# Kernel tuning notes

Hardware: AMD Instinct MI355X
Metric: run time of the kernel (lower is better)

The kernel has to match this reference:

```python
import jax, jax.numpy as jnp
import numpy as np
from jax import lax

FEAT_STRIDE = 16
SCALES = (8, 16, 32)
RATIOS = (0.5, 1.0, 2.0)
PRE_NMS = 6000
POST_NMS = 300
NMS_THRESH = 0.7
MIN_SIZE = 16.0


def _base_anchors():
    base = 16.0
    cx = cy = base / 2.0
    anchors = []
    for r in RATIOS:
        for s in SCALES:
            h = base * s * np.sqrt(r)
            w = base * s * np.sqrt(1.0 / r)
            anchors.append([cx - w / 2, cy - h / 2, cx + w / 2, cy + h / 2])
    return np.asarray(anchors, np.float32)  # [A,4] (x1,y1,x2,y2)


def _shifted_anchors(h, w):
    base = _base_anchors()
    sy = np.arange(h, dtype=np.float32) * FEAT_STRIDE
    sx = np.arange(w, dtype=np.float32) * FEAT_STRIDE
    yy, xx = np.meshgrid(sy, sx, indexing='ij')  # h-major then w, matching NHWC permute
    shifts = np.stack([xx, yy, xx, yy], axis=-1).reshape(-1, 1, 4)
    return (shifts + base[None]).reshape(-1, 4).astype(np.float32)  # [h*w*A,4]


def _conv(x, w, b, pad):
    y = lax.conv_general_dilated(x, w, (1, 1), [(pad, pad), (pad, pad)],
                                 dimension_numbers=('NCHW', 'OIHW', 'NCHW'))
    return y + b[None, :, None, None]


def _iou(box, boxes):
    lt = jnp.maximum(box[:2], boxes[:, :2])
    rb = jnp.minimum(box[2:], boxes[:, 2:])
    wh = jnp.maximum(rb - lt, 0.0)
    inter = wh[:, 0] * wh[:, 1]
    a1 = (box[2] - box[0]) * (box[3] - box[1])
    a2 = (boxes[:, 2] - boxes[:, 0]) * (boxes[:, 3] - boxes[:, 1])
    return inter / (a1 + a2 - inter + 1e-9)


def _nms_proposals(boxes, scores):
    # boxes [K,4], scores [K] -> [POST_NMS,4]
    ws = boxes[:, 2] - boxes[:, 0]
    hs = boxes[:, 3] - boxes[:, 1]
    scores = jnp.where((ws >= MIN_SIZE) & (hs >= MIN_SIZE), scores, -jnp.inf)
    top_s, idx = lax.top_k(scores, PRE_NMS)
    b = boxes[idx]

    def body(i, st):
        keep, s = st
        j = jnp.argmax(s).astype(jnp.int32)
        keep = keep.at[i].set(j)
        sup = _iou(b[j], b) >= NMS_THRESH  # suppresses j itself too (iou=1)
        s = jnp.where(sup, -jnp.inf, s)
        return keep, s

    keep, _ = lax.fori_loop(0, POST_NMS, body,
                            (jnp.zeros((POST_NMS,), jnp.int32), top_s))
    return b[keep]


def setup_inputs() -> dict:
    key = jax.random.key(0)
    ks = jax.random.split(key, 5)
    n, c, h, w = 8, 512, 50, 64
    A = len(SCALES) * len(RATIOS)
    x = jax.random.normal(ks[0], (n, c, h, w), jnp.float32)
    w1 = jax.random.normal(ks[1], (512, 512, 3, 3), jnp.float32) * 0.02
    b1 = jnp.zeros((512,), jnp.float32)
    w_cls = jax.random.normal(ks[2], (A * 2, 512, 1, 1), jnp.float32) * 0.02
    b_cls = jnp.zeros((A * 2,), jnp.float32)
    w_bbox = jax.random.normal(ks[3], (A * 4, 512, 1, 1), jnp.float32) * 0.005
    b_bbox = jnp.zeros((A * 4,), jnp.float32)
    return {'x': x, 'w1': w1, 'b1': b1, 'w_cls': w_cls, 'b_cls': b_cls,
            'w_bbox': w_bbox, 'b_bbox': b_bbox}


def reference(x, w1, b1, w_cls, b_cls, w_bbox, b_bbox):
    n, _, h, w = x.shape
    A = len(SCALES) * len(RATIOS)
    img_h, img_w = h * FEAT_STRIDE, w * FEAT_STRIDE
    anchors = jnp.asarray(_shifted_anchors(h, w))  # [h*w*A,4]

    feat = jax.nn.relu(_conv(x, w1, b1, 1))
    cls = _conv(feat, w_cls, b_cls, 0).transpose(0, 2, 3, 1).reshape(n, h, w, A, 2)
    fg = jax.nn.softmax(cls, axis=-1)[..., 1].reshape(n, -1)  # [n, h*w*A]
    deltas = _conv(feat, w_bbox, b_bbox, 0).transpose(0, 2, 3, 1).reshape(n, -1, 4)

    # decode deltas against anchors
    aw = anchors[:, 2] - anchors[:, 0]
    ah = anchors[:, 3] - anchors[:, 1]
    acx = anchors[:, 0] + 0.5 * aw
    acy = anchors[:, 1] + 0.5 * ah
    cx = deltas[..., 0] * aw + acx
    cy = deltas[..., 1] * ah + acy
    pw = jnp.exp(deltas[..., 2]) * aw
    ph = jnp.exp(deltas[..., 3]) * ah
    boxes = jnp.stack([cx - 0.5 * pw, cy - 0.5 * ph,
                       cx + 0.5 * pw, cy + 0.5 * ph], axis=-1)  # [n,K,4]
    hi = jnp.asarray([img_w, img_h, img_w, img_h], jnp.float32)
    boxes = jnp.clip(boxes, 0.0, hi)

    rois = jax.vmap(_nms_proposals)(boxes, fg)  # [n,POST_NMS,4]
    roi_indices = jnp.repeat(jnp.arange(n, dtype=jnp.int32), POST_NMS)
    return rois.reshape(-1, 4), roi_indices
```

## Files before the change

### kernel.cpp

```cpp
#include <hip/hip_runtime.h>
#include <math.h>

#define NIMG 8
#define CIN  512
#define HF   50
#define WF   64
#define HW   3200
#define NA   9
#define KPER 28800
#define PRE  6000
#define POST 300

#define WHT_ELEMS  32768

#define NW    94
#define NCAP  6016
#define NTRI  4465

#define XTROWS 52
#define XTCOLS 66
#define XT_ELEMS ((size_t)NIMG * XTROWS * XTCOLS * CIN)
#define XT_BYTES (XT_ELEMS * 2)

#define WPK_ELEMS ((size_t)2 * 4 * 9 * 16 * 4096)
#define WPK_HALF  (4 * 9 * 16 * 4096)

#define SCALE_X 256.0f
#define SCALE_W 16384.0f
#define INV_SCALE (1.0f / 4194304.0f)

#define PB_XT   1600
#define PB_HALO 64
#define PB_WPK  288
#define PB_PH   16
#define PB_TOT  (PB_XT + PB_HALO + PB_WPK + PB_PH)

#define HALO_VPI 14848
#define HALO_TOT (NIMG * HALO_VPI)

typedef _Float16 f16x8 __attribute__((ext_vector_type(8)));
typedef float f32x4  __attribute__((ext_vector_type(4)));
typedef unsigned short u16x8 __attribute__((ext_vector_type(8)));
typedef unsigned long long u64;

__constant__ float BASEA[9][4] = {
  {-82.509667991878083f, -37.254833995939042f,  98.509667991878083f,  53.254833995939042f},
  {-173.01933598375617f, -82.509667991878083f, 189.01933598375617f,   98.509667991878083f},
  {-354.03867196751233f, -173.01933598375617f, 370.03867196751233f,  189.01933598375617f},
  { -56.0f,  -56.0f,  72.0f,  72.0f},
  {-120.0f, -120.0f, 136.0f, 136.0f},
  {-248.0f, -248.0f, 264.0f, 264.0f},
  {-37.254833995939042f, -82.509667991878083f,  53.254833995939042f,  98.509667991878083f},
  {-82.509667991878083f, -173.01933598375617f,  98.509667991878083f, 189.01933598375617f},
  {-173.01933598375617f, -354.03867196751233f, 189.01933598375617f,  370.03867196751233f},
};

__device__ __forceinline__ unsigned int ordf(float f) {
  unsigned int u = __float_as_uint(f);
  return (u & 0x80000000u) ? ~u : (u | 0x80000000u);
}

__device__ __forceinline__ unsigned short f2h(float f) {
  union { _Float16 h; unsigned short u; } cv;
  cv.h = (_Float16)f;
  return cv.u;
}
__device__ __forceinline__ float h2f(unsigned short u) {
  union { _Float16 h; unsigned short u; } cv;
  cv.u = u;
  return (float)cv.h;
}

__global__ __launch_bounds__(256) void k_prep_all(
    const float4* __restrict__ x4,
    const float* __restrict__ w1,
    const float* __restrict__ wc, const float* __restrict__ bc,
    const float* __restrict__ wb, const float* __restrict__ bb,
    unsigned short* __restrict__ xh, unsigned short* __restrict__ xl,
    unsigned short* __restrict__ wpk,
    float* __restrict__ WHT2, float* __restrict__ bh) {
  __shared__ float tile[128][65];
  const int blk = blockIdx.x;
  const int t = threadIdx.x;

  if (blk < PB_XT) {
    const int cic = blk & 3;
    const int rest = blk >> 2;
    const int hrow = rest % 50;
    const int n = rest / 50;
#pragma unroll
    for (int jj = 0; jj < 8; ++jj) {
      const int e = t + 256 * jj;
      const int row = e >> 4, c4 = e & 15;
      const float4 v = x4[(((size_t)(n * CIN + cic * 128 + row) * HF + hrow) << 4) + c4];
      tile[row][c4 * 4 + 0] = v.x;
      tile[row][c4 * 4 + 1] = v.y;
      tile[row][c4 * 4 + 2] = v.z;
      tile[row][c4 * 4 + 3] = v.w;
    }
    __syncthreads();
#pragma unroll
    for (int jj = 0; jj < 4; ++jj) {
      const int e = t + 256 * jj;
      const int w = e >> 4, c8 = e & 15;
      const size_t base = ((size_t)((n * XTROWS + (hrow + 1)) * XTCOLS) + (w + 1)) * CIN
                          + cic * 128 + c8 * 8;
      u16x8 hv, lv;
#pragma unroll
      for (int u = 0; u < 8; ++u) {
        const float g = tile[c8 * 8 + u][w] * SCALE_X;
        const unsigned short hh = f2h(g);
        hv[u] = (short)hh;
        lv[u] = (short)f2h(g - h2f(hh));
      }
      *reinterpret_cast<u16x8*>(xh + base) = hv;
      *reinterpret_cast<u16x8*>(xl + base) = lv;
    }
  } else if (blk < PB_XT + PB_HALO) {
    const u16x8 z = {0, 0, 0, 0, 0, 0, 0, 0};
    const int tid = (blk - PB_XT) * 256 + t;
    for (int v = tid; v < HALO_TOT; v += PB_HALO * 256) {
      const int n = v / HALO_VPI;
      const int r = v - n * HALO_VPI;
      int row, col, v8;
      if (r < 8448) {
        row = (r < 4224) ? 0 : 51;
        const int r2 = (r < 4224) ? r : r - 4224;
        col = r2 >> 6;
        v8 = r2 & 63;
      } else {
        const int q = r - 8448;
        row = 1 + (q >> 7);
        const int rr = q & 127;
        col = (rr >= 64) ? 65 : 0;
        v8 = rr & 63;
      }
      const size_t off = ((size_t)((n * XTROWS + row) * XTCOLS) + col) * CIN + v8 * 8;
      *reinterpret_cast<u16x8*>(xh + off) = z;
      *reinterpret_cast<u16x8*>(xl + off) = z;
    }
  } else if (blk < PB_XT + PB_HALO + PB_WPK) {
    const int tot = (int)WPK_ELEMS;
    const int tid = (blk - PB_XT - PB_HALO) * 256 + t;
    for (int idx = tid; idx < tot; idx += PB_WPK * 256) {
      const int i = idx & 4095;
      int rest = idx >> 12;
      const int ks = rest & 15; rest >>= 4;
      const int tap = rest % 9; rest /= 9;
      const int cob = rest & 3;
      const int sp = rest >> 2;
      const int col = i >> 5;
      const int slotp = (i >> 3) & 3;
      const int j = i & 7;
      const int s = slotp ^ ((col >> 1) & 3);
      const int ci = ks * 32 + s * 8 + j;
      const int co = cob * 128 + col;
      const float g = w1[((size_t)co * CIN + ci) * 9 + tap] * SCALE_W;
      const unsigned short hh = f2h(g);
      wpk[idx] = sp ? f2h(g - h2f(hh)) : hh;
    }
  } else {
    const int TOT = WHT_ELEMS + 64;
    const int tid = (blk - PB_XT - PB_HALO - PB_WPK) * 256 + t;
    for (int idx = tid; idx < TOT; idx += PB_PH * 256) {
      if (idx < WHT_ELEMS) {
        int r = idx & 3;
        int o = (idx >> 2) & 63;
        int c = (idx >> 8) * 4 + r;
        float v = 0.0f;
        if (o < 18) v = wc[(size_t)o * CIN + c];
        else if (o < 54) v = wb[(size_t)(o - 18) * CIN + c];
        WHT2[idx] = v;
      } else {
        int o = idx - WHT_ELEMS;
        float v = 0.0f;
        if (o < 18) v = bc[o];
        else if (o < 54) v = bb[o - 18];
        bh[o] = v;
      }
    }
  }
}

#define GLDS(gp, lp) __builtin_amdgcn_global_load_lds( \
    (const __attribute__((address_space(1))) unsigned int*)(gp), \
    (__attribute__((address_space(3))) unsigned int*)(lp), 16, 0, 0)

__global__ __launch_bounds__(256, 2) void k_convmfma(
    const unsigned short* __restrict__ xh,
    const unsigned short* __restrict__ xl,
    const unsigned short* __restrict__ wpk,
    const float* __restrict__ b1,
    float* __restrict__ feat) {
  __shared__ unsigned short lds[2][4][4096];

  const int raw = blockIdx.x;
  const int xcd = raw & 7;
  const int idx = raw >> 3;
  const int cob = xcd >> 1;
  const int pb  = (xcd & 1) * 100 + idx;

  const int n   = pb / 25;
  const int h0  = (pb - n * 25) * 2;
  const int t   = threadIdx.x;
  const int wid = t >> 6;
  const int l   = t & 63;
  const int wm  = wid >> 1;
  const int wn  = wid & 1;

  const int colp = l >> 2;
  const int sB = (((l & 3) ^ ((l >> 3) & 3)) << 3);
  const unsigned short* xsrc = (wid == 3) ? xl : xh;
  const size_t wA_base = (size_t)(wid & 1) * WPK_HALF;

  const int fr = l & 15;
  const int fq = l >> 4;
  const int slotr = ((fq ^ ((fr >> 1) & 3)) << 4);

  f32x4 acc[4][4] = {};

  auto stage = [&](int sbuf, int ti) {
    const int ks  = ti / 9;
    const int tap = ti - ks * 9;
    if (wid < 2) {
      const unsigned short* gp = wpk + wA_base
          + ((size_t)((cob * 9 + tap) * 16 + ks) << 12) + l * 8;
      unsigned short* lp = &lds[sbuf][wid][0];
#pragma unroll
      for (int q = 0; q < 8; ++q)
        GLDS(gp + q * 512, lp + q * 512);
    } else {
      const int ky = (tap * 11) >> 5;
      const int kx = tap - ky * 3;
      const size_t ebase = ((size_t)((n * XTROWS + h0 + ky) * XTCOLS + kx + colp) << 9)
                           + ks * 32 + sB;
      unsigned short* lp = &lds[sbuf][wid][0];
#pragma unroll
      for (int q = 0; q < 8; ++q)
        GLDS(xsrc + ebase + ((size_t)(((q >> 2) * XTCOLS + (q & 3) * 16)) << 9),
             lp + q * 512);
    }
  };

  stage(0, 0);
  __syncthreads();

  int buf = 0;
  for (int ti = 0; ti < 144; ++ti) {
    if (ti < 143) stage(buf ^ 1, ti + 1);

    f16x8 ah[4], al[4], bhf[4], blf[4];
#pragma unroll
    for (int mi = 0; mi < 4; ++mi) {
      const int off = (((wm << 6) + (mi << 4) + fr) << 6) + slotr;
      ah[mi] = *(const f16x8*)((const char*)&lds[buf][0][0] + off);
      al[mi] = *(const f16x8*)((const char*)&lds[buf][1][0] + off);
    }
#pragma unroll
    for (int ni = 0; ni < 4; ++ni) {
      const int off = (((wn << 6) + (ni << 4) + fr) << 6) + slotr;
      bhf[ni] = *(const f16x8*)((const char*)&lds[buf][2][0] + off);
      blf[ni] = *(const f16x8*)((const char*)&lds[buf][3][0] + off);
    }
#pragma unroll
    for (int mi = 0; mi < 4; ++mi)
#pragma unroll
      for (int ni = 0; ni < 4; ++ni) {
        acc[mi][ni] = __builtin_amdgcn_mfma_f32_16x16x32_f16(ah[mi], bhf[ni], acc[mi][ni], 0, 0, 0);
        acc[mi][ni] = __builtin_amdgcn_mfma_f32_16x16x32_f16(ah[mi], blf[ni], acc[mi][ni], 0, 0, 0);
        acc[mi][ni] = __builtin_amdgcn_mfma_f32_16x16x32_f16(al[mi], bhf[ni], acc[mi][ni], 0, 0, 0);
      }
    __syncthreads();
    buf ^= 1;
  }

  const int h = h0 + wn;
#pragma unroll
  for (int mi = 0; mi < 4; ++mi) {
    const int co = (cob << 7) + (wm << 6) + (mi << 4) + (fq << 2);
    const float4 bias = *(const float4*)&b1[co];
#pragma unroll
    for (int ni = 0; ni < 4; ++ni) {
      const int w = (ni << 4) + fr;
      float4 v;
      v.x = fmaxf(fmaf(acc[mi][ni][0], INV_SCALE, bias.x), 0.0f);
      v.y = fmaxf(fmaf(acc[mi][ni][1], INV_SCALE, bias.y), 0.0f);
      v.z = fmaxf(fmaf(acc[mi][ni][2], INV_SCALE, bias.z), 0.0f);
      v.w = fmaxf(fmaf(acc[mi][ni][3], INV_SCALE, bias.w), 0.0f);
      *(float4*)(feat + (((size_t)n * HW + h * WF + w) << 9) + co) = v;
    }
  }
}

__global__ __launch_bounds__(256) void k_head(const float* __restrict__ feat,
                                              const float* __restrict__ WHT2,
                                              const float* __restrict__ bh,
                                              float* __restrict__ scores,
                                              float4* __restrict__ boxes) {
  __shared__ float fsh[16][512];
  __shared__ float vsh[16][64];
  const int t = threadIdx.x;
  const int wvid = t >> 6;
  const int o = t & 63;
  const int pos0 = blockIdx.x * 16;

  for (int i = t; i < 16 * 512; i += 256)
    fsh[i >> 9][i & 511] = feat[((size_t)pos0 << 9) + i];
  __syncthreads();

  {
    const int p0 = wvid * 4;
    float a0 = 0.f, a1 = 0.f, a2 = 0.f, a3 = 0.f;
    const float4* wp = reinterpret_cast<const float4*>(WHT2);
    const float4* f0 = reinterpret_cast<const float4*>(&fsh[p0 + 0][0]);
    const float4* f1 = reinterpret_cast<const float4*>(&fsh[p0 + 1][0]);
    const float4* f2 = reinterpret_cast<const float4*>(&fsh[p0 + 2][0]);
    const float4* f3 = reinterpret_cast<const float4*>(&fsh[p0 + 3][0]);
#pragma unroll 4
    for (int c4 = 0; c4 < 128; ++c4) {
      float4 w4 = wp[c4 * 64 + o];
      float4 v;
      v = f0[c4];
      a0 = fmaf(w4.x, v.x, a0); a0 = fmaf(w4.y, v.y, a0);
      a0 = fmaf(w4.z, v.z, a0); a0 = fmaf(w4.w, v.w, a0);
      v = f1[c4];
      a1 = fmaf(w4.x, v.x, a1); a1 = fmaf(w4.y, v.y, a1);
      a1 = fmaf(w4.z, v.z, a1); a1 = fmaf(w4.w, v.w, a1);
      v = f2[c4];
      a2 = fmaf(w4.x, v.x, a2); a2 = fmaf(w4.y, v.y, a2);
      a2 = fmaf(w4.z, v.z, a2); a2 = fmaf(w4.w, v.w, a2);
      v = f3[c4];
      a3 = fmaf(w4.x, v.x, a3); a3 = fmaf(w4.y, v.y, a3);
      a3 = fmaf(w4.z, v.z, a3); a3 = fmaf(w4.w, v.w, a3);
    }
    float bv = bh[o];
    vsh[p0 + 0][o] = a0 + bv;
    vsh[p0 + 1][o] = a1 + bv;
    vsh[p0 + 2][o] = a2 + bv;
    vsh[p0 + 3][o] = a3 + bv;
  }
  __syncthreads();

  if (t < 144) {
    const int p2 = t / 9, a = t % 9;
    const int pos = pos0 + p2;
    const int n = pos / HW;
    const int r = pos - n * HW;
    const int ph = r >> 6;
    const int pw = r & 63;

    float l0 = vsh[p2][a * 2];
    float l1 = vsh[p2][a * 2 + 1];
    float m  = fmaxf(l0, l1);
    float e0 = (float)exp((double)__fsub_rn(l0, m));
    float e1 = (float)exp((double)__fsub_rn(l1, m));
    float fg = __fdiv_rn(e1, __fadd_rn(e0, e1));

    float d0 = vsh[p2][18 + a * 4 + 0];
    float d1 = vsh[p2][18 + a * 4 + 1];
    float d2 = vsh[p2][18 + a * 4 + 2];
    float d3 = vsh[p2][18 + a * 4 + 3];

    float sx = (float)(pw * 16);
    float sy = (float)(ph * 16);
    float ax1 = __fadd_rn(BASEA[a][0], sx);
    float ay1 = __fadd_rn(BASEA[a][1], sy);
    float ax2 = __fadd_rn(BASEA[a][2], sx);
    float ay2 = __fadd_rn(BASEA[a][3], sy);
    float aw = __fsub_rn(ax2, ax1);
    float ah = __fsub_rn(ay2, ay1);
    float acx = __fadd_rn(ax1, __fmul_rn(0.5f, aw));
    float acy = __fadd_rn(ay1, __fmul_rn(0.5f, ah));
    float cx = __fadd_rn(__fmul_rn(d0, aw), acx);
    float cy = __fadd_rn(__fmul_rn(d1, ah), acy);
    float pwd = __fmul_rn((float)exp((double)d2), aw);
    float phd = __fmul_rn((float)exp((double)d3), ah);
    float x1 = __fsub_rn(cx, __fmul_rn(0.5f, pwd));
    float y1 = __fsub_rn(cy, __fmul_rn(0.5f, phd));
    float x2 = __fadd_rn(cx, __fmul_rn(0.5f, pwd));
    float y2 = __fadd_rn(cy, __fmul_rn(0.5f, phd));
    x1 = fminf(fmaxf(x1, 0.0f), 1024.0f);
    x2 = fminf(fmaxf(x2, 0.0f), 1024.0f);
    y1 = fminf(fmaxf(y1, 0.0f), 800.0f);
    y2 = fminf(fmaxf(y2, 0.0f), 800.0f);
    float wsz = __fsub_rn(x2, x1);
    float hsz = __fsub_rn(y2, y1);
    float sc = (wsz >= 16.0f && hsz >= 16.0f) ? fg : -__builtin_huge_valf();

    const int idx = n * KPER + r * NA + a;
    scores[idx] = sc;
    boxes[idx] = make_float4(x1, y1, x2, y2);
  }
}

__global__ __launch_bounds__(1024) void k_select(const float* __restrict__ scores,
                                                 const float4* __restrict__ boxes,
                                                 float4* __restrict__ sbox,
                                                 u64* __restrict__ valid) {
  __shared__ u64 sk[8192];
  __shared__ unsigned int hist[256];
  __shared__ unsigned int sh_selB, sh_ngt, sh_binc, sh_num;
  const int n = blockIdx.x;
  const int t = threadIdx.x;
  const float* sc = scores + (size_t)n * KPER;

  for (int e = t; e < 8192; e += 1024) sk[e] = 0ull;

  unsigned int prefix = 0, prefMask = 0, ngt = 0, neq = 0;
  for (int shift = 24; shift >= 0; shift -= 8) {
    if (t < 256) hist[t] = 0;
    __syncthreads();
    for (int i = t; i < KPER; i += 1024) {
      unsigned int u = ordf(sc[i]);
      if ((u & prefMask) == prefix) atomicAdd(&hist[(u >> shift) & 255], 1u);
    }
    __syncthreads();
    if (t == 0) {
      unsigned int cnt = ngt;
      for (int b = 255; b >= 0; --b) {
        unsigned int c = hist[b];
        if (cnt + c >= (unsigned)PRE) { sh_selB = (unsigned)b; sh_ngt = cnt; sh_binc = c; break; }
        cnt += c;
      }
    }
    __syncthreads();
    prefix |= (sh_selB << shift);
    prefMask |= (0xFFu << shift);
    ngt = sh_ngt;
    neq = sh_binc;
    __syncthreads();
  }
  const unsigned int T = prefix;
  const unsigned int needed = (unsigned)PRE - ngt;
  unsigned int J = 0xFFFFFFFFu;
  if (needed < neq) {
    if (t < 256) hist[t] = 0;
    __syncthreads();
    for (int i = t; i < KPER; i += 1024)
      if (ordf(sc[i]) == T) atomicAdd(&hist[i >> 7], 1u);
    __syncthreads();
    if (t == 0) {
      unsigned int cnt = 0;
      for (int b = 0; b < 256; ++b) {
        unsigned int c = hist[b];
        if (cnt + c >= needed) { sh_selB = (unsigned)b; sh_ngt = needed - cnt; break; }
        cnt += c;
      }
    }
    __syncthreads();
    const unsigned int selH = sh_selB;
    const unsigned int needLow = sh_ngt;
    __syncthreads();
    if (t < 128) hist[t] = 0;
    __syncthreads();
    for (int i = t; i < KPER; i += 1024)
      if (ordf(sc[i]) == T && ((unsigned)(i >> 7)) == selH) atomicAdd(&hist[i & 127], 1u);
    __syncthreads();
    if (t == 0) {
      unsigned int cnt = 0;
      for (int b = 0; b < 128; ++b) {
        unsigned int c = hist[b];
        if (cnt + c >= needLow) { sh_selB = (selH << 7) | (unsigned)b; break; }
        cnt += c;
      }
    }
    __syncthreads();
    J = sh_selB;
  }

  if (t == 0) sh_num = 0;
  __syncthreads();
  for (int i = t; i < KPER; i += 1024) {
    unsigned int u = ordf(sc[i]);
    bool in = (u > T) || (u == T && (unsigned)i <= J);
    if (in) {
      unsigned int p = atomicAdd(&sh_num, 1u);
      sk[p] = (((u64)u) << 32) | (u64)(~(unsigned int)i);
    }
  }
  __syncthreads();

  for (int k = 2; k <= 8192; k <<= 1) {
    for (int j = k >> 1; j > 0; j >>= 1) {
      for (int p = t; p < 4096; p += 1024) {
        const int i = ((p & ~(j - 1)) << 1) | (p & (j - 1));
        const int ip = i | j;
        u64 a = sk[i], b = sk[ip];
        const bool desc = ((i & k) == 0);
        if ((a < b) == desc) { sk[i] = b; sk[ip] = a; }
      }
      __syncthreads();
    }
  }

  for (int e = t; e < NCAP; e += 1024) {
    float4 bx = make_float4(0.f, 0.f, 0.f, 0.f);
    if (e < PRE) {
      unsigned idx = ~(unsigned)(sk[e] & 0xFFFFFFFFull);
      bx = boxes[(size_t)n * KPER + idx];
    }
    sbox[(size_t)n * NCAP + e] = bx;
  }
  if (t < 128) {
    u64 w = 0;
    if (t < NW) {
      for (int b = 0; b < 64; ++b) {
        int e = t * 64 + b;
        if (e < PRE && ((sk[e] >> 32) > 0x007FFFFFull)) w |= 1ull << b;
      }
    }
    valid[n * 128 + t] = w;
  }
}

__global__ __launch_bounds__(64) void k_mask(const float4* __restrict__ sbox,
                                             u64* __restrict__ mask) {
  const int p = blockIdx.x;
  const int n = blockIdx.y;
  int ib = (int)((189.0 - sqrt(35721.0 - 8.0 * (double)p)) * 0.5);
  while (94 * (ib + 1) - (ib * (ib + 1)) / 2 <= p) ++ib;
  while (94 * ib - ((ib - 1) * ib) / 2 > p) --ib;
  const int jb = ib + (p - (94 * ib - ((ib - 1) * ib) / 2));

  const int r = threadIdx.x;
  const int i = ib * 64 + r;
  __shared__ float4 jbox[64];
  jbox[r] = sbox[(size_t)n * NCAP + jb * 64 + r];
  __syncthreads();
  const float4 pbx = sbox[(size_t)n * NCAP + i];
  const float pa = __fmul_rn(__fsub_rn(pbx.z, pbx.x), __fsub_rn(pbx.w, pbx.y));
  u64 word = 0;
#pragma unroll 8
  for (int b = 0; b < 64; ++b) {
    const float4 q = jbox[b];
    float ltx = fmaxf(pbx.x, q.x);
    float lty = fmaxf(pbx.y, q.y);
    float rbx = fminf(pbx.z, q.z);
    float rby = fminf(pbx.w, q.w);
    float wv = fmaxf(__fsub_rn(rbx, ltx), 0.0f);
    float hv = fmaxf(__fsub_rn(rby, lty), 0.0f);
    float inter = __fmul_rn(wv, hv);
    float a2 = __fmul_rn(__fsub_rn(q.z, q.x), __fsub_rn(q.w, q.y));
    float denom = __fadd_rn(__fsub_rn(__fadd_rn(pa, a2), inter), 1e-9f);
    float iou = __fdiv_rn(inter, denom);
    if (iou >= 0.7f) word |= (1ull << b);
  }
  mask[((size_t)(n * NCAP) + i) * NW + jb] = word;
}

__global__ __launch_bounds__(64) void k_scan(const u64* __restrict__ mask,
                                             const u64* __restrict__ valid,
                                             const float4* __restrict__ sbox,
                                             float* __restrict__ out) {
  const int n = blockIdx.x;
  const int lane = threadIdx.x;
  u64 s0 = 0, s1 = 0;
  const u64 v0 = valid[n * 128 + 2 * lane];
  const u64 v1 = valid[n * 128 + 2 * lane + 1];
  const u64* mrow = mask + (size_t)n * NCAP * NW;
  __shared__ int keep_list[POST];
  int kept = 0;

  ulonglong2 cur[16], nxt[16];
#pragma unroll
  for (int r = 0; r < 16; ++r)
    cur[r] = ((const ulonglong2*)(mrow + (size_t)r * NW))[lane];

  for (int g = 0; g < PRE / 16; ++g) {
    if (kept >= POST) break;
    if (g < PRE / 16 - 1) {
#pragma unroll
      for (int r = 0; r < 16; ++r)
        nxt[r] = ((const ulonglong2*)(mrow + (size_t)((g + 1) * 16 + r) * NW))[lane];
    }
#pragma unroll
    for (int r = 0; r < 16; ++r) {
      if (kept < POST) {
        const int i = g * 16 + r;
        const int w = i >> 6;
        const u64 avail = (w & 1) ? (v1 & ~s1) : (v0 & ~s0);
        const unsigned h32 = (unsigned)(avail >> (i & 32));
        const unsigned wrd = __shfl(h32, w >> 1, 64);
        if ((wrd >> (i & 31)) & 1u) {
          if (lane == 0) keep_list[kept] = i;
          ++kept;
          s0 |= cur[r].x;
          s1 |= cur[r].y;
        }
      }
    }
#pragma unroll
    for (int r = 0; r < 16; ++r) cur[r] = nxt[r];
  }
  __syncthreads();

  for (int it = lane; it < POST; it += 64) {
    const int cand = (it < kept) ? keep_list[it] : 0;
    const float4 b = sbox[(size_t)n * NCAP + cand];
    float* orow = out + ((size_t)n * POST + it) * 4;
    orow[0] = b.x; orow[1] = b.y; orow[2] = b.z; orow[3] = b.w;
    out[(size_t)NIMG * POST * 4 + (size_t)n * POST + it] = (float)n;
  }
}

extern "C" void kernel_launch(void* const* d_in, const int* in_sizes, int n_in,
                              void* d_out, int out_size, void* d_ws, size_t ws_size,
                              hipStream_t stream) {
  const float* x    = (const float*)d_in[0];
  const float* w1   = (const float*)d_in[1];
  const float* b1   = (const float*)d_in[2];
  const float* wcls = (const float*)d_in[3];
  const float* bcls = (const float*)d_in[4];
  const float* wbb  = (const float*)d_in[5];
  const float* bbb  = (const float*)d_in[6];
  float* out = (float*)d_out;

  char* ws = (char*)d_ws;
  size_t off = 0;
  float* feat = (float*)(ws + off);               off += (size_t)NIMG * HW * CIN * 4;
  float* scores = (float*)(ws + off);             off += (size_t)NIMG * KPER * 4;
  float4* boxes = (float4*)(ws + off);            off += (size_t)NIMG * KPER * 16;
  float4* sbox = (float4*)(ws + off);             off += (size_t)NIMG * NCAP * 16;
  u64* valid = (u64*)(ws + off);                  off += (size_t)NIMG * 128 * 8;
  u64* mask = (u64*)(ws + off);                   off += (size_t)NIMG * NCAP * NW * 8;
  float* WHT2 = (float*)(ws + off);               off += (size_t)WHT_ELEMS * 4;
  float* bh   = (float*)(ws + off);               off += 256;
  unsigned short* xTh = (unsigned short*)(ws + off); off += XT_BYTES;
  unsigned short* xTl = (unsigned short*)(ws + off); off += XT_BYTES;
  unsigned short* wpk = (unsigned short*)(ws + off); off += WPK_ELEMS * 2;

  k_prep_all<<<PB_TOT, 256, 0, stream>>>((const float4*)x, w1, wcls, bcls, wbb, bbb,
                                         xTh, xTl, wpk, WHT2, bh);
  k_convmfma<<<800, 256, 0, stream>>>(xTh, xTl, wpk, b1, feat);
  k_head<<<(NIMG * HW) / 16, 256, 0, stream>>>(feat, WHT2, bh, scores, boxes);
  k_select<<<NIMG, 1024, 0, stream>>>(scores, boxes, sbox, valid);
  k_mask<<<dim3(NTRI, NIMG), 64, 0, stream>>>(sbox, mask);
  k_scan<<<NIMG, 64, 0, stream>>>(mask, valid, sbox, out);
}
```

Measured before the change: 756.6 us.

## Fuse top-k selection, IoU suppression and scan into one per-image NMS kernel

Replaces the separate select, pairwise IoU bitmask, and serial scan kernels with a single block-per-image kernel. It keeps the sorted candidate boxes in registers and performs greedy NMS iteratively, recomputing IoU against the picked box each step with ballot-based suppression bits in shared memory. This removes the large mask buffer and two launches, but uses only one block per image and needs several barriers for each of up to 300 iterations.

```diff
diff --git a/kernel.cpp b/kernel.cpp
--- a/kernel.cpp
+++ b/kernel.cpp
@@ -14,8 +14,6 @@
 #define WHT_ELEMS  32768
 
 #define NW    94
-#define NCAP  6016
-#define NTRI  4465
 
 #define XTROWS 52
 #define XTCOLS 66
@@ -393,13 +391,19 @@
   }
 }
 
-__global__ __launch_bounds__(1024) void k_select(const float* __restrict__ scores,
-                                                 const float4* __restrict__ boxes,
-                                                 float4* __restrict__ sbox,
-                                                 u64* __restrict__ valid) {
+__global__ __launch_bounds__(1024) void k_nms_fused(const float* __restrict__ scores,
+                                                    const float4* __restrict__ boxes,
+                                                    float* __restrict__ out) {
   __shared__ u64 sk[8192];
+  __shared__ int sidx[6144];
   __shared__ unsigned int hist[256];
   __shared__ unsigned int sh_selB, sh_ngt, sh_binc, sh_num;
+  __shared__ u64 validw[96], supp[96];
+  __shared__ int cand_arr[128];
+  __shared__ int keep_list[POST];
+  __shared__ int next_sh;
+  __shared__ float4 pick_sh;
+
   const int n = blockIdx.x;
   const int t = threadIdx.x;
   const float* sc = scores + (size_t)n * KPER;
@@ -493,15 +497,9 @@
     }
   }
 
-  for (int e = t; e < NCAP; e += 1024) {
-    float4 bx = make_float4(0.f, 0.f, 0.f, 0.f);
-    if (e < PRE) {
-      unsigned idx = ~(unsigned)(sk[e] & 0xFFFFFFFFull);
-      bx = boxes[(size_t)n * KPER + idx];
-    }
-    sbox[(size_t)n * NCAP + e] = bx;
-  }
-  if (t < 128) {
+  for (int e = t; e < 6144; e += 1024)
+    sidx[e] = (e < PRE) ? (int)(~(unsigned)(sk[e] & 0xFFFFFFFFull)) : -1;
+  if (t < 96) {
     u64 w = 0;
     if (t < NW) {
       for (int b = 0; b < 64; ++b) {
@@ -509,94 +507,77 @@
         if (e < PRE && ((sk[e] >> 32) > 0x007FFFFFull)) w |= 1ull << b;
       }
     }
-    valid[n * 128 + t] = w;
-  }
-}
-
-__global__ __launch_bounds__(64) void k_mask(const float4* __restrict__ sbox,
-                                             u64* __restrict__ mask) {
-  const int p = blockIdx.x;
-  const int n = blockIdx.y;
-  int ib = (int)((189.0 - sqrt(35721.0 - 8.0 * (double)p)) * 0.5);
-  while (94 * (ib + 1) - (ib * (ib + 1)) / 2 <= p) ++ib;
-  while (94 * ib - ((ib - 1) * ib) / 2 > p) --ib;
-  const int jb = ib + (p - (94 * ib - ((ib - 1) * ib) / 2));
-
-  const int r = threadIdx.x;
-  const int i = ib * 64 + r;
-  __shared__ float4 jbox[64];
-  jbox[r] = sbox[(size_t)n * NCAP + jb * 64 + r];
+    validw[t] = w;
+    supp[t] = 0ull;
+  }
   __syncthreads();
-  const float4 pbx = sbox[(size_t)n * NCAP + i];
-  const float pa = __fmul_rn(__fsub_rn(pbx.z, pbx.x), __fsub_rn(pbx.w, pbx.y));
-  u64 word = 0;
-#pragma unroll 8
-  for (int b = 0; b < 64; ++b) {
-    const float4 q = jbox[b];
-    float ltx = fmaxf(pbx.x, q.x);
-    float lty = fmaxf(pbx.y, q.y);
-    float rbx = fminf(pbx.z, q.z);
-    float rby = fminf(pbx.w, q.w);
-    float wv = fmaxf(__fsub_rn(rbx, ltx), 0.0f);
-    float hv = fmaxf(__fsub_rn(rby, lty), 0.0f);
-    float inter = __fmul_rn(wv, hv);
-    float a2 = __fmul_rn(__fsub_rn(q.z, q.x), __fsub_rn(q.w, q.y));
-    float denom = __fadd_rn(__fsub_rn(__fadd_rn(pa, a2), inter), 1e-9f);
-    float iou = __fdiv_rn(inter, denom);
-    if (iou >= 0.7f) word |= (1ull << b);
-  }
-  mask[((size_t)(n * NCAP) + i) * NW + jb] = word;
-}
-
-__global__ __launch_bounds__(64) void k_scan(const u64* __restrict__ mask,
-                                             const u64* __restrict__ valid,
-                                             const float4* __restrict__ sbox,
-                                             float* __restrict__ out) {
-  const int n = blockIdx.x;
-  const int lane = threadIdx.x;
-  u64 s0 = 0, s1 = 0;
-  const u64 v0 = valid[n * 128 + 2 * lane];
-  const u64 v1 = valid[n * 128 + 2 * lane + 1];
-  const u64* mrow = mask + (size_t)n * NCAP * NW;
-  __shared__ int keep_list[POST];
+
+  float4 myb[6];
+#pragma unroll
+  for (int s = 0; s < 6; ++s) {
+    const int e = t + s * 1024;
+    float4 bx = make_float4(0.f, 0.f, 0.f, 0.f);
+    if (e < PRE) bx = boxes[(size_t)n * KPER + sidx[e]];
+    myb[s] = bx;
+  }
+  const int wv = t >> 6;
+  const int lane = t & 63;
+
   int kept = 0;
-
-  ulonglong2 cur[16], nxt[16];
-#pragma unroll
-  for (int r = 0; r < 16; ++r)
-    cur[r] = ((const ulonglong2*)(mrow + (size_t)r * NW))[lane];
-
-  for (int g = 0; g < PRE / 16; ++g) {
-    if (kept >= POST) break;
-    if (g < PRE / 16 - 1) {
-#pragma unroll
-      for (int r = 0; r < 16; ++r)
-        nxt[r] = ((const ulonglong2*)(mrow + (size_t)((g + 1) * 16 + r) * NW))[lane];
-    }
-#pragma unroll
-    for (int r = 0; r < 16; ++r) {
-      if (kept < POST) {
-        const int i = g * 16 + r;
-        const int w = i >> 6;
-        const u64 avail = (w & 1) ? (v1 & ~s1) : (v0 & ~s0);
-        const unsigned h32 = (unsigned)(avail >> (i & 32));
-        const unsigned wrd = __shfl(h32, w >> 1, 64);
-        if ((wrd >> (i & 31)) & 1u) {
-          if (lane == 0) keep_list[kept] = i;
-          ++kept;
-          s0 |= cur[r].x;
-          s1 |= cur[r].y;
-        }
-      }
-    }
-#pragma unroll
-    for (int r = 0; r < 16; ++r) cur[r] = nxt[r];
+  for (int iter = 0; iter < POST; ++iter) {
+    int c = 0x7FFFFFFF;
+    if (t < 96) {
+      u64 w = validw[t] & ~supp[t];
+      if (w) c = t * 64 + (int)__builtin_ctzll(w);
+    }
+    if (t < 128) cand_arr[t] = c;
+    __syncthreads();
+    if (t < 64) {
+      int a = cand_arr[t] < cand_arr[t + 64] ? cand_arr[t] : cand_arr[t + 64];
+#pragma unroll
+      for (int off = 32; off; off >>= 1) {
+        int b = __shfl_down(a, off, 64);
+        if (b < a) a = b;
+      }
+      if (t == 0) next_sh = a;
+    }
+    __syncthreads();
+    const int pick = next_sh;
+    if (pick == 0x7FFFFFFF) break;
+    if (t == (pick & 1023)) {
+      const int sl = pick >> 10;
+#pragma unroll
+      for (int q = 0; q < 6; ++q)
+        if (q == sl) pick_sh = myb[q];
+    }
+    if (t == 0) keep_list[iter] = pick;
+    __syncthreads();
+    const float4 p = pick_sh;
+    const float pa = __fmul_rn(__fsub_rn(p.z, p.x), __fsub_rn(p.w, p.y));
+#pragma unroll
+    for (int s = 0; s < 6; ++s) {
+      const float4 q = myb[s];
+      float ltx = fmaxf(p.x, q.x);
+      float lty = fmaxf(p.y, q.y);
+      float rbx = fminf(p.z, q.z);
+      float rby = fminf(p.w, q.w);
+      float wvv = fmaxf(__fsub_rn(rbx, ltx), 0.0f);
+      float hvv = fmaxf(__fsub_rn(rby, lty), 0.0f);
+      float inter = __fmul_rn(wvv, hvv);
+      float a2 = __fmul_rn(__fsub_rn(q.z, q.x), __fsub_rn(q.w, q.y));
+      float denom = __fadd_rn(__fsub_rn(__fadd_rn(pa, a2), inter), 1e-9f);
+      float iou = __fdiv_rn(inter, denom);
+      u64 bal = __ballot(iou >= 0.7f);
+      if (lane == 0) supp[wv + 16 * s] |= bal;
+    }
+    ++kept;
+    __syncthreads();
   }
   __syncthreads();
 
-  for (int it = lane; it < POST; it += 64) {
+  for (int it = t; it < POST; it += 1024) {
     const int cand = (it < kept) ? keep_list[it] : 0;
-    const float4 b = sbox[(size_t)n * NCAP + cand];
+    const float4 b = boxes[(size_t)n * KPER + sidx[cand]];
     float* orow = out + ((size_t)n * POST + it) * 4;
     orow[0] = b.x; orow[1] = b.y; orow[2] = b.z; orow[3] = b.w;
     out[(size_t)NIMG * POST * 4 + (size_t)n * POST + it] = (float)n;
@@ -620,9 +601,6 @@
   float* feat = (float*)(ws + off);               off += (size_t)NIMG * HW * CIN * 4;
   float* scores = (float*)(ws + off);             off += (size_t)NIMG * KPER * 4;
   float4* boxes = (float4*)(ws + off);            off += (size_t)NIMG * KPER * 16;
-  float4* sbox = (float4*)(ws + off);             off += (size_t)NIMG * NCAP * 16;
-  u64* valid = (u64*)(ws + off);                  off += (size_t)NIMG * 128 * 8;
-  u64* mask = (u64*)(ws + off);                   off += (size_t)NIMG * NCAP * NW * 8;
   float* WHT2 = (float*)(ws + off);               off += (size_t)WHT_ELEMS * 4;
   float* bh   = (float*)(ws + off);               off += 256;
   unsigned short* xTh = (unsigned short*)(ws + off); off += XT_BYTES;
@@ -633,7 +611,5 @@
                                          xTh, xTl, wpk, WHT2, bh);
   k_convmfma<<<800, 256, 0, stream>>>(xTh, xTl, wpk, b1, feat);
   k_head<<<(NIMG * HW) / 16, 256, 0, stream>>>(feat, WHT2, bh, scores, boxes);
-  k_select<<<NIMG, 1024, 0, stream>>>(scores, boxes, sbox, valid);
-  k_mask<<<dim3(NTRI, NIMG), 64, 0, stream>>>(sbox, mask);
-  k_scan<<<NIMG, 64, 0, stream>>>(mask, valid, sbox, out);
-}
+  k_nms_fused<<<NIMG, 1024, 0, stream>>>(scores, boxes, out);
+}
```

New measurement: 1.156 ms. +52.8%, slower.
